# Kernel tuning notes

Measured on AMD Instinct MI355X. Metric: run time of the kernel, lower is better.

The kernel has to match this reference:

```python
import jax, jax.numpy as jnp
import numpy as np

E4M3_MAX = 448.0  # max representable value of float8_e4m3fn


def _updated_scale(amax_history, amax_now, scale):
    # roll history, insert current amax, take running max (delayed scaling)
    hist = jnp.roll(amax_history, 1).at[0].set(amax_now)
    amax = jnp.max(hist)
    sf = E4M3_MAX / amax  # scale factor (margin = 0)
    sf = jnp.where((amax > 0.0) & jnp.isfinite(amax), sf, 1.0 / scale)
    return 1.0 / sf  # dequant scale


def _qdq(x, scale, amax_history):
    # quantize-dequantize through float8_e4m3fn with dynamic amax-history scaling
    amax_now = jnp.max(jnp.abs(x)).astype(jnp.float32)
    s = _updated_scale(amax_history, amax_now, scale[0])
    q = jnp.clip(x / s, -E4M3_MAX, E4M3_MAX).astype(jnp.float8_e4m3fn)
    return q.astype(x.dtype) * s


def setup_inputs() -> dict:
    key = jax.random.key(0)
    k1, k2 = jax.random.split(key, 2)
    B, S, D, F = 4, 2048, 4096, 16384
    HL = 16  # amax_history_length
    inputs = jax.random.normal(k1, (B, S, D), jnp.float32)
    # lecun_normal: std = 1/sqrt(fan_in)
    kernel = jax.random.normal(k2, (D, F), jnp.float32) * (1.0 / np.sqrt(D))
    bias = jnp.zeros((F,), jnp.float32)
    return {
        "inputs": inputs,
        "kernel": kernel,
        "bias": bias,
        "input_scale": jnp.ones((1,), jnp.float32),
        "input_amax_history": jnp.zeros((HL,), jnp.float32),
        "kernel_scale": jnp.ones((1,), jnp.float32),
        "kernel_amax_history": jnp.zeros((HL,), jnp.float32),
        "output_grad_scale": jnp.ones((1,), jnp.float32),
        "output_grad_amax_history": jnp.zeros((HL,), jnp.float32),
    }


def reference(inputs, kernel, bias, input_scale, input_amax_history,
              kernel_scale, kernel_amax_history, output_grad_scale,
              output_grad_amax_history):
    B, S, D = inputs.shape
    x = inputs.reshape(-1, D)  # (B*S, D)
    q_x = _qdq(x, input_scale, input_amax_history)
    q_k = _qdq(kernel, kernel_scale, kernel_amax_history)
    out = q_x @ q_k  # (B*S, F)
    # bias is rounded fp32->bf16->fp32 per the module
    b = bias.astype(jnp.bfloat16).astype(jnp.float32)
    out = jax.nn.gelu(out + b)
    return out.reshape(B, S, -1)
```

## Files before the change

### kernel.cpp

```cpp
#include <hip/hip_runtime.h>
#include <hip/hip_bf16.h>

typedef __attribute__((ext_vector_type(4))) int i32x4;
typedef __attribute__((ext_vector_type(8))) int i32x8;
typedef __attribute__((ext_vector_type(16))) float f32x16;

#define E4M3_MAX 448.0f
#define AS1 __attribute__((address_space(1)))
#define AS3 __attribute__((address_space(3)))

__device__ __forceinline__ float clip448(float v) {
  return fminf(fmaxf(v, -E4M3_MAX), E4M3_MAX);
}

__device__ __forceinline__ void gld_lds16(const void* g, void* l) {
  __builtin_amdgcn_global_load_lds((const AS1 void*)g, (AS3 void*)l, 16, 0, 0);
}

__device__ __forceinline__ float gelu_f(float v) {
  float y = 0.7978845608028654f * (v + 0.044715f * v * v * v);
  float a = fabsf(y);
  float z = __expf(-2.f * a);
  float th = (1.f - z) / (1.f + z);
  th = copysignf(th, y);
  return 0.5f * v * (1.f + th);
}

__global__ void init_ws_kernel(unsigned int* amax) {
  amax[0] = 0u;
  amax[1] = 0u;
}

__global__ void amax_kernel(const float* __restrict__ x, long n4,
                            unsigned int* __restrict__ amax_out) {
  long i0 = (long)blockIdx.x * blockDim.x + threadIdx.x;
  long stride = (long)gridDim.x * blockDim.x;
  const float4* x4 = (const float4*)x;
  float m = 0.f;
  for (long i = i0; i < n4; i += stride) {
    float4 v = x4[i];
    m = fmaxf(m, fmaxf(fmaxf(fabsf(v.x), fabsf(v.y)), fmaxf(fabsf(v.z), fabsf(v.w))));
  }
#pragma unroll
  for (int off = 32; off >= 1; off >>= 1)
    m = fmaxf(m, __shfl_xor(m, off));
  __shared__ float wmax[8];
  int wid = threadIdx.x >> 6;
  if ((threadIdx.x & 63) == 0) wmax[wid] = m;
  __syncthreads();
  if (threadIdx.x == 0) {
    int nw = blockDim.x >> 6;
    float bm = wmax[0];
    for (int w = 1; w < nw; ++w) bm = fmaxf(bm, wmax[w]);
    atomicMax(amax_out, __float_as_uint(bm));
  }
}

__global__ void scale_kernel(const unsigned int* __restrict__ amax,
                             const float* __restrict__ scale_x,
                             const float* __restrict__ hist_x,
                             const float* __restrict__ scale_k,
                             const float* __restrict__ hist_k,
                             int hl, float* __restrict__ scales) {
  if (threadIdx.x != 0) return;
  float ax = __uint_as_float(amax[0]);
  for (int i = 0; i < hl - 1; ++i) ax = fmaxf(ax, hist_x[i]);
  float sfx = E4M3_MAX / ax;
  if (!(ax > 0.f && isfinite(ax))) sfx = 1.f / scale_x[0];
  float sx = 1.f / sfx;
  float ak = __uint_as_float(amax[1]);
  for (int i = 0; i < hl - 1; ++i) ak = fmaxf(ak, hist_k[i]);
  float sfk = E4M3_MAX / ak;
  if (!(ak > 0.f && isfinite(ak))) sfk = 1.f / scale_k[0];
  float sk = 1.f / sfk;
  scales[0] = sx;
  scales[1] = sk;
  scales[2] = sx * sk;
}


__global__ void quant_x_kernel(const float* __restrict__ x,
                               unsigned char* __restrict__ Aq,
                               const float* __restrict__ scales, int K) {
  const float s = scales[0];
  const int kt = blockIdx.x, mt = blockIdx.y, nkt = gridDim.x;
  __shared__ float lt[128][68];
  const int t = threadIdx.x;
  const float* src = x + (size_t)mt * 128 * K + (size_t)kt * 64;
#pragma unroll
  for (int it = 0; it < 8; ++it) {
    int row = it * 16 + (t >> 4);
    int c4 = (t & 15) * 4;
    float4 v = *(const float4*)&src[(size_t)row * K + c4];
    lt[row][c4 + 0] = v.x; lt[row][c4 + 1] = v.y;
    lt[row][c4 + 2] = v.z; lt[row][c4 + 3] = v.w;
  }
  __syncthreads();
  uint4* out = (uint4*)(Aq + ((size_t)mt * nkt + kt) * 8192);
#pragma unroll
  for (int cc = 0; cc < 2; ++cc) {
    int c = t * 2 + cc;
    int g = c >> 7, h = (c >> 6) & 1, l = c & 63;
    int row = g * 32 + (l & 31);
    int kb = (l >> 5) * 32 + h * 16;
    unsigned int w[4];
#pragma unroll
    for (int q = 0; q < 4; ++q) {
      int b = kb + q * 4;
      int p = 0;
      p = __builtin_amdgcn_cvt_pk_fp8_f32(clip448(lt[row][b+0] / s), clip448(lt[row][b+1] / s), p, false);
      p = __builtin_amdgcn_cvt_pk_fp8_f32(clip448(lt[row][b+2] / s), clip448(lt[row][b+3] / s), p, true);
      w[q] = (unsigned int)p;
    }
    out[c] = make_uint4(w[0], w[1], w[2], w[3]);
  }
}

__global__ void quant_k_kernel(const float* __restrict__ w,
                               unsigned char* __restrict__ Bq,
                               const float* __restrict__ scales, int N) {
  const float s = scales[1];
  const int kt = blockIdx.x, nt = blockIdx.y, nkt = gridDim.x;
  __shared__ float lt[64][132];
  const int t = threadIdx.x;
  const float* src = w + (size_t)kt * 64 * N + (size_t)nt * 128;
#pragma unroll
  for (int it = 0; it < 8; ++it) {
    int row = it * 8 + (t >> 5);
    int c4 = (t & 31) * 4;
    float4 v = *(const float4*)&src[(size_t)row * N + c4];
    lt[row][c4 + 0] = v.x; lt[row][c4 + 1] = v.y;
    lt[row][c4 + 2] = v.z; lt[row][c4 + 3] = v.w;
  }
  __syncthreads();
  uint4* out = (uint4*)(Bq + ((size_t)nt * nkt + kt) * 8192);
#pragma unroll
  for (int cc = 0; cc < 2; ++cc) {
    int c = t * 2 + cc;
    int g = c >> 7, h = (c >> 6) & 1, l = c & 63;
    int nl = g * 32 + (l & 31);
    int kb = (l >> 5) * 32 + h * 16;
    unsigned int w4[4];
#pragma unroll
    for (int q = 0; q < 4; ++q) {
      int b = kb + q * 4;
      int p = 0;
      p = __builtin_amdgcn_cvt_pk_fp8_f32(clip448(lt[b+0][nl] / s), clip448(lt[b+1][nl] / s), p, false);
      p = __builtin_amdgcn_cvt_pk_fp8_f32(clip448(lt[b+2][nl] / s), clip448(lt[b+3][nl] / s), p, true);
      w4[q] = (unsigned int)p;
    }
    out[c] = make_uint4(w4[0], w4[1], w4[2], w4[3]);
  }
}

#define BUFSZ 32768

#define RD_AV(dst, g_)                                                         \
  {                                                                            \
    const unsigned char* p_ =                                                  \
        lds + cb + ((g_) >> 2) * 8192 + ((g_) & 3) * 2048 + lane * 16;         \
    i32x4 lo_ = *(const i32x4*)p_;                                             \
    i32x4 hi_ = *(const i32x4*)(p_ + 1024);                                    \
    dst = __builtin_shufflevector(lo_, hi_, 0, 1, 2, 3, 4, 5, 6, 7);           \
  }
#define RD_BV(dst, g_)                                                         \
  {                                                                            \
    const unsigned char* p_ =                                                  \
        lds + cb + 16384 + ((g_) >> 2) * 8192 + ((g_) & 3) * 2048 + lane * 16; \
    i32x4 lo_ = *(const i32x4*)p_;                                             \
    i32x4 hi_ = *(const i32x4*)(p_ + 1024);                                    \
    dst = __builtin_shufflevector(lo_, hi_, 0, 1, 2, 3, 4, 5, 6, 7);           \
  }
#define MFMA1(r_, c_, a_, b_)                                                  \
  acc[r_][c_] = __builtin_amdgcn_mfma_scale_f32_32x32x64_f8f6f4(               \
      a_, b_, acc[r_][c_], 0, 0, 0, 127, 0, 127);

__global__ __launch_bounds__(512, 2) void gemm_fp8_kernel(
    const unsigned char* __restrict__ Aq, const unsigned char* __restrict__ Bq,
    const float* __restrict__ bias, const float* __restrict__ scales,
    float* __restrict__ C, int M, int N, int K) {
  __shared__ __align__(16) unsigned char lds[3 * BUFSZ];
  const float s_xk = scales[2];
  const int nkt = K >> 6;
  const int t = threadIdx.x;
  const int lane = t & 63;
  const int wid = t >> 6;
  const int wm = wid >> 2, wn = wid & 3;

  int f = blockIdx.y * gridDim.x + blockIdx.x;
  int cpx = (gridDim.x * gridDim.y) >> 3;
  int f2 = (f & 7) * cpx + (f >> 3);
  int bx = f2 % gridDim.x;
  int by = f2 / gridDim.x;

  const size_t strideT = (size_t)nkt * 8192;
  const unsigned char* gA = Aq + (size_t)(2 * by) * strideT + t * 16;
  const unsigned char* gB = Bq + (size_t)(2 * bx) * strideT + t * 16;

  f32x16 acc[4][2];
#pragma unroll
  for (int i = 0; i < 4; ++i)
#pragma unroll
    for (int j = 0; j < 2; ++j)
#pragma unroll
      for (int r = 0; r < 16; ++r) acc[i][j][r] = 0.f;

  auto stageA = [&](unsigned bufbase, int kt_) {
    size_t o = (size_t)kt_ * 8192;
    unsigned char* l = lds + bufbase + wid * 1024;
    gld_lds16(gA + o,           l);
    gld_lds16(gA + strideT + o, l + 8192);
  };
  auto stageB = [&](unsigned bufbase, int kt_) {
    size_t o = (size_t)kt_ * 8192;
    unsigned char* l = lds + bufbase + 16384 + wid * 1024;
    gld_lds16(gB + o,           l);
    gld_lds16(gB + strideT + o, l + 8192);
  };

  i32x8 av0, av1, av2, av3, bv0, bv1;

  stageA(0, 0); stageB(0, 0);
  stageA(BUFSZ, 1); stageB(BUFSZ, 1);
  asm volatile("s_waitcnt vmcnt(4)" ::: "memory");
  __builtin_amdgcn_s_barrier();

  unsigned cb = 0;
  for (int kt = 0; kt < nkt; ++kt) {
    unsigned sb = cb + 2 * BUFSZ;
    if (sb >= 3 * BUFSZ) sb -= 3 * BUFSZ;
    const bool st = (kt + 2 < nkt);

    RD_AV(av0, wm * 4 + 0);
    RD_AV(av1, wm * 4 + 1);
    RD_BV(bv0, wn * 2 + 0);
    RD_BV(bv1, wn * 2 + 1);
    if (st) stageA(sb, kt + 2);
    __builtin_amdgcn_s_barrier();
    asm volatile("s_waitcnt lgkmcnt(0)" ::: "memory");
    __builtin_amdgcn_s_setprio(1);
    MFMA1(0, 0, av0, bv0); MFMA1(0, 1, av0, bv1);
    MFMA1(1, 0, av1, bv0); MFMA1(1, 1, av1, bv1);
    __builtin_amdgcn_s_setprio(0);
    __builtin_amdgcn_s_barrier();

    RD_AV(av2, wm * 4 + 2);
    RD_AV(av3, wm * 4 + 3);
    if (st) {
      stageB(sb, kt + 2);
      asm volatile("s_waitcnt vmcnt(4)" ::: "memory");
    } else if (kt + 1 < nkt) {
      asm volatile("s_waitcnt vmcnt(0)" ::: "memory");
    }
    __builtin_amdgcn_s_barrier();
    asm volatile("s_waitcnt lgkmcnt(0)" ::: "memory");
    __builtin_amdgcn_s_setprio(1);
    MFMA1(2, 0, av2, bv0); MFMA1(2, 1, av2, bv1);
    MFMA1(3, 0, av3, bv0); MFMA1(3, 1, av3, bv1);
    __builtin_amdgcn_s_setprio(0);
    __builtin_amdgcn_s_barrier();

    cb += BUFSZ;
    if (cb == 3 * BUFSZ) cb = 0;
  }

  const int m0 = by * 256;
  const int n0 = bx * 256;
  float bb[2];
#pragma unroll
  for (int j = 0; j < 2; ++j) {
    int col = n0 + wn * 64 + j * 32 + (lane & 31);
    bb[j] = __bfloat162float(__float2bfloat16(bias[col]));
  }
#pragma unroll
  for (int i = 0; i < 4; ++i) {
    int rowbase = m0 + wm * 128 + i * 32 + 4 * (lane >> 5);
#pragma unroll
    for (int j = 0; j < 2; ++j) {
      int col = n0 + wn * 64 + j * 32 + (lane & 31);
#pragma unroll
      for (int r = 0; r < 16; ++r) {
        int row = rowbase + (r & 3) + 8 * (r >> 2);
        float v = acc[i][j][r] * s_xk + bb[j];
        __builtin_nontemporal_store(gelu_f(v), &C[(size_t)row * N + col]);
      }
    }
  }
}

extern "C" void kernel_launch(void* const* d_in, const int* in_sizes, int n_in,
                              void* d_out, int out_size, void* d_ws, size_t ws_size,
                              hipStream_t stream) {
  const float* inputs = (const float*)d_in[0];
  const float* kernelw = (const float*)d_in[1];
  const float* bias = (const float*)d_in[2];
  const float* input_scale = (const float*)d_in[3];
  const float* input_hist = (const float*)d_in[4];
  const float* kernel_scale = (const float*)d_in[5];
  const float* kernel_hist = (const float*)d_in[6];

  const int F = in_sizes[2];
  const int D = in_sizes[1] / F;
  const long M = (long)in_sizes[0] / D;
  const int HL = in_sizes[4];
  const int N = F, K = D;

  unsigned int* amax = (unsigned int*)d_ws;
  float* scales = (float*)((char*)d_ws + 16);
  unsigned char* Aq = (unsigned char*)d_ws + 64;
  unsigned char* Bq = Aq + (size_t)M * K;

  float* C = (float*)d_out;

  init_ws_kernel<<<1, 1, 0, stream>>>(amax);
  amax_kernel<<<2048, 256, 0, stream>>>(inputs, (long)M * K / 4, &amax[0]);
  amax_kernel<<<2048, 256, 0, stream>>>(kernelw, (long)K * N / 4, &amax[1]);
  scale_kernel<<<1, 64, 0, stream>>>(amax, input_scale, input_hist, kernel_scale,
                                     kernel_hist, HL, scales);
  quant_x_kernel<<<dim3(K / 64, M / 128), 256, 0, stream>>>(inputs, Aq, scales, K);
  quant_k_kernel<<<dim3(K / 64, N / 128), 256, 0, stream>>>(kernelw, Bq, scales, N);
  gemm_fp8_kernel<<<dim3(N / 256, M / 256), 512, 0, stream>>>(Aq, Bq, bias, scales, C,
                                                              (int)M, N, K);
}
```

Before: 756.5 us.

## Restructure FP8 GEMM main loop to four LDS buffers with one barrier per step

The K loop moves from a three-buffer ring, with A and B staged in separate half-steps and four barriers per iteration, to a four-buffer ring. Each iteration now stages A and B for tile kt+2 together, waits on vmcnt, hits a single barrier, reads all LDS fragments and issues all eight MFMAs. The aim is to cut barrier and synchronisation overhead and let the compiler schedule LDS reads and MFMAs more freely. In exchange, the setprio hints and the interleaving of LDS reads with MFMA halves are gone. LDS use grows by a third, which may limit the two-blocks-per-CU occupancy.

```diff
diff --git a/kernel.cpp b/kernel.cpp
--- a/kernel.cpp
+++ b/kernel.cpp
@@ -179,7 +179,7 @@
     const unsigned char* __restrict__ Aq, const unsigned char* __restrict__ Bq,
     const float* __restrict__ bias, const float* __restrict__ scales,
     float* __restrict__ C, int M, int N, int K) {
-  __shared__ __align__(16) unsigned char lds[3 * BUFSZ];
+  __shared__ __align__(16) unsigned char lds[4 * BUFSZ];
   const float s_xk = scales[2];
   const int nkt = K >> 6;
   const int t = threadIdx.x;
@@ -205,63 +205,45 @@
 #pragma unroll
       for (int r = 0; r < 16; ++r) acc[i][j][r] = 0.f;
 
-  auto stageA = [&](unsigned bufbase, int kt_) {
+  auto stage = [&](unsigned bufbase, int kt_) {
     size_t o = (size_t)kt_ * 8192;
     unsigned char* l = lds + bufbase + wid * 1024;
     gld_lds16(gA + o,           l);
     gld_lds16(gA + strideT + o, l + 8192);
+    gld_lds16(gB + o,           l + 16384);
+    gld_lds16(gB + strideT + o, l + 24576);
   };
-  auto stageB = [&](unsigned bufbase, int kt_) {
-    size_t o = (size_t)kt_ * 8192;
-    unsigned char* l = lds + bufbase + 16384 + wid * 1024;
-    gld_lds16(gB + o,           l);
-    gld_lds16(gB + strideT + o, l + 8192);
-  };
 
   i32x8 av0, av1, av2, av3, bv0, bv1;
 
-  stageA(0, 0); stageB(0, 0);
-  stageA(BUFSZ, 1); stageB(BUFSZ, 1);
-  asm volatile("s_waitcnt vmcnt(4)" ::: "memory");
-  __builtin_amdgcn_s_barrier();
-
-  unsigned cb = 0;
+  stage(0 * BUFSZ, 0);
+  stage(1 * BUFSZ, 1);
+
   for (int kt = 0; kt < nkt; ++kt) {
-    unsigned sb = cb + 2 * BUFSZ;
-    if (sb >= 3 * BUFSZ) sb -= 3 * BUFSZ;
-    const bool st = (kt + 2 < nkt);
-
-    RD_AV(av0, wm * 4 + 0);
-    RD_AV(av1, wm * 4 + 1);
-    RD_BV(bv0, wn * 2 + 0);
-    RD_BV(bv1, wn * 2 + 1);
-    if (st) stageA(sb, kt + 2);
-    __builtin_amdgcn_s_barrier();
-    asm volatile("s_waitcnt lgkmcnt(0)" ::: "memory");
-    __builtin_amdgcn_s_setprio(1);
-    MFMA1(0, 0, av0, bv0); MFMA1(0, 1, av0, bv1);
-    MFMA1(1, 0, av1, bv0); MFMA1(1, 1, av1, bv1);
-    __builtin_amdgcn_s_setprio(0);
-    __builtin_amdgcn_s_barrier();
-
-    RD_AV(av2, wm * 4 + 2);
-    RD_AV(av3, wm * 4 + 3);
-    if (st) {
-      stageB(sb, kt + 2);
+    const unsigned cb = (kt & 3) * BUFSZ;
+
+    if (kt + 2 < nkt) {
+      stage(((kt + 2) & 3) * BUFSZ, kt + 2);
+      asm volatile("s_waitcnt vmcnt(8)" ::: "memory");
+    } else if (kt + 1 < nkt) {
       asm volatile("s_waitcnt vmcnt(4)" ::: "memory");
-    } else if (kt + 1 < nkt) {
+    } else {
       asm volatile("s_waitcnt vmcnt(0)" ::: "memory");
     }
     __builtin_amdgcn_s_barrier();
-    asm volatile("s_waitcnt lgkmcnt(0)" ::: "memory");
-    __builtin_amdgcn_s_setprio(1);
+    asm volatile("" ::: "memory");
+
+    RD_AV(av0, wm * 4 + 0);
+    RD_BV(bv0, wn * 2 + 0);
+    RD_BV(bv1, wn * 2 + 1);
+    RD_AV(av1, wm * 4 + 1);
+    RD_AV(av2, wm * 4 + 2);
+    RD_AV(av3, wm * 4 + 3);
+
+    MFMA1(0, 0, av0, bv0); MFMA1(0, 1, av0, bv1);
+    MFMA1(1, 0, av1, bv0); MFMA1(1, 1, av1, bv1);
     MFMA1(2, 0, av2, bv0); MFMA1(2, 1, av2, bv1);
     MFMA1(3, 0, av3, bv0); MFMA1(3, 1, av3, bv1);
-    __builtin_amdgcn_s_setprio(0);
-    __builtin_amdgcn_s_barrier();
-
-    cb += BUFSZ;
-    if (cb == 3 * BUFSZ) cb = 0;
   }
 
   const int m0 = by * 256;
```

Result: faster. 730.6 us, median of 2 (-3.4%).
